# Kernel optimization log

Measured on AMD Instinct MI355X. Metric: run time of the kernel, lower is better.

The kernel has to match this reference:

```python
import jax, jax.numpy as jnp
import numpy as np

B, S, HID = 1, 2048, 2048
NH, NKV, HD = 16, 4, 128
ROPE_BASE = 10000.0


def _rope(q, k, positions):
    # q: [B,NH,S,HD], k: [B,NKV,S,HD]; rotate-half RoPE
    half = HD // 2
    inv_freq = 1.0 / (ROPE_BASE ** (jnp.arange(half, dtype=jnp.float32) / half))
    ang = positions.astype(jnp.float32)[:, None] * inv_freq  # [S, half]
    cos, sin = jnp.cos(ang), jnp.sin(ang)

    def apply(x):
        x1, x2 = x[..., :half], x[..., half:]
        return jnp.concatenate([x1 * cos - x2 * sin, x1 * sin + x2 * cos], axis=-1)

    return apply(q), apply(k)


def setup_inputs() -> dict:
    key = jax.random.key(0)
    ks = jax.random.split(key, 5)
    hidden_states = jax.random.normal(ks[0], (B, S, HID), dtype=jnp.float32)
    positions = jnp.arange(S, dtype=jnp.int32)
    # additive causal mask (finite large negative instead of -inf)
    mask = jnp.triu(jnp.full((S, S), -1e9, dtype=jnp.float32), k=1)[None, None]
    scale = 0.02
    Wq = jax.random.normal(ks[1], (HID, NH * HD), dtype=jnp.float32) * scale
    Wk = jax.random.normal(ks[2], (HID, NKV * HD), dtype=jnp.float32) * scale
    Wv = jax.random.normal(ks[3], (HID, NKV * HD), dtype=jnp.float32) * scale
    Wo = jax.random.normal(ks[4], (NH * HD, HID), dtype=jnp.float32) * scale
    return {"hidden_states": hidden_states, "positions": positions, "mask": mask,
            "Wq": Wq, "Wk": Wk, "Wv": Wv, "Wo": Wo}


def reference(hidden_states, positions, mask, Wq, Wk, Wv, Wo):
    groups = NH // NKV
    q = (hidden_states @ Wq).reshape(B, S, NH, HD).transpose(0, 2, 1, 3)
    k = (hidden_states @ Wk).reshape(B, S, NKV, HD).transpose(0, 2, 1, 3)
    v = (hidden_states @ Wv).reshape(B, S, NKV, HD).transpose(0, 2, 1, 3)
    q, k = _rope(q, k, positions)
    # GQA: duplicate kv heads (repeat_interleave along head dim)
    k = jnp.repeat(k, groups, axis=1)
    v = jnp.repeat(v, groups, axis=1)
    scale = 1.0 / jnp.sqrt(jnp.float32(HD))
    scores = jnp.einsum('bhqd,bhkd->bhqk', q, k) * scale + mask
    attn = jax.nn.softmax(scores.astype(jnp.float32), axis=-1).astype(q.dtype)
    out = jnp.einsum('bhqk,bhkd->bhqd', attn, v)
    out = out.transpose(0, 2, 1, 3).reshape(B, S, NH * HD)
    output = out @ Wo
    return (output, k, v)
```

## Files before the change

kernel.cpp:

```cpp
#include <hip/hip_runtime.h>
#include <hip/hip_bf16.h>
#include <math.h>

#define S_LEN 2048
#define HID_DIM 2048
#define NH 16
#define NKV 4
#define HD 128

typedef __attribute__((ext_vector_type(8))) short bf16x8;
typedef __attribute__((ext_vector_type(4))) float f32x4;

#define AS1 __attribute__((address_space(1)))
#define AS3 __attribute__((address_space(3)))

__device__ inline unsigned short f2bf(float f) {
  unsigned int u = __float_as_uint(f);
  unsigned int r = u + 0x7FFFu + ((u >> 16) & 1u);
  return (unsigned short)(r >> 16);
}
__device__ inline float bf2f(unsigned short u) {
  return __uint_as_float(((unsigned int)u) << 16);
}

__global__ __launch_bounds__(256) void transpose_all(
    const float* __restrict__ Wq, const float* __restrict__ Wk,
    const float* __restrict__ Wv, const float* __restrict__ Wo,
    unsigned short* __restrict__ WT, unsigned short* __restrict__ WoT,
    const float* __restrict__ hidden, unsigned short* __restrict__ h_bf)
{
  const int z = blockIdx.z;
  if (z == 4) {
    int bb = blockIdx.y * 64 + blockIdx.x;
    int t = threadIdx.y * 32 + threadIdx.x;
    int i = (bb * 256 + t) * 4;
    float4 v = *(const float4*)&hidden[i];
    ushort4 o;
    o.x = f2bf(v.x); o.y = f2bf(v.y); o.z = f2bf(v.z); o.w = f2bf(v.w);
    *(ushort4*)&h_bf[i] = o;
    return;
  }
  __shared__ float t[32][33];
  const float* W; unsigned short* D; int N;
  if (z == 0)      { W = Wq; D = WT;                          N = 2048; }
  else if (z == 1) { W = Wk; D = WT + (size_t)2048 * 2048;    N = 512;  }
  else if (z == 2) { W = Wv; D = WT + (size_t)2560 * 2048;    N = 512;  }
  else             { W = Wo; D = WoT;                         N = 2048; }
  int bx = blockIdx.x * 32;
  if (bx >= N) return;
  int by = blockIdx.y * 32;
  int tx = threadIdx.x, ty = threadIdx.y;
  #pragma unroll
  for (int i = 0; i < 32; i += 8)
    t[ty + i][tx] = W[(size_t)(by + ty + i) * N + bx + tx];
  __syncthreads();
  #pragma unroll
  for (int i = 0; i < 32; i += 8)
    D[(size_t)(bx + ty + i) * 2048 + by + tx] = f2bf(t[tx][ty + i]);
}

__global__ __launch_bounds__(512) void gemm_bt_8phase(
    const unsigned short* __restrict__ A,
    const unsigned short* __restrict__ Bt,
    unsigned short* __restrict__ P,
    int M, int N, int KF, int ksplit)
{
  extern __shared__ unsigned short smem[];
  unsigned short* Ab = smem;
  unsigned short* Bb = smem + 32768;
  const int bm = blockIdx.y * 256, bn = blockIdx.x * 256, z = blockIdx.z;
  const int Kh = KF / ksplit, k0z = z * Kh;
  const int NT = Kh >> 6;
  const int tid = threadIdx.x, lane = tid & 63, wave = tid >> 6;
  const int wm = wave >> 2, wn = wave & 3;
  const int quad = lane >> 4, lcol = lane & 15;

  auto stageA = [&](int t, int kh) {
    const unsigned short* src = A + (size_t)bm * KF + k0z + t * 64 + kh * 32;
    unsigned short* dst = Ab + (((t & 1) * 2 + kh) << 13);
    #pragma unroll
    for (int i = 0; i < 2; i++) {
      int s = i * 512 + tid;
      int row = s >> 2, dc = s & 3, g = dc ^ ((row >> 1) & 3);
      __builtin_amdgcn_global_load_lds(
          (const AS1 void*)(src + (size_t)row * KF + g * 8),
          (AS3 void*)(dst + s * 8), 16, 0, 0);
    }
  };
  auto stageB = [&](int t, int kh) {
    const unsigned short* src = Bt + (size_t)bn * KF + k0z + t * 64 + kh * 32;
    unsigned short* dst = Bb + (((t & 1) * 2 + kh) << 13);
    #pragma unroll
    for (int i = 0; i < 2; i++) {
      int s = i * 512 + tid;
      int row = s >> 2, dc = s & 3, g = dc ^ ((row >> 1) & 3);
      __builtin_amdgcn_global_load_lds(
          (const AS1 void*)(src + (size_t)row * KF + g * 8),
          (AS3 void*)(dst + s * 8), 16, 0, 0);
    }
  };
  auto ldA = [&](int cur, int kh, int mh, bf16x8* af) {
    const unsigned short* base = Ab + ((cur * 2 + kh) << 13);
    #pragma unroll
    for (int m = 0; m < 4; m++) {
      int row = wm * 128 + (mh * 4 + m) * 16 + lcol;
      int ch = quad ^ ((row >> 1) & 3);
      af[m] = *(const bf16x8*)&base[row * 32 + ch * 8];
    }
  };
  auto ldB = [&](int cur, int kh, bf16x8* bfr) {
    const unsigned short* base = Bb + ((cur * 2 + kh) << 13);
    #pragma unroll
    for (int n = 0; n < 4; n++) {
      int row = wn * 64 + n * 16 + lcol;
      int ch = quad ^ ((row >> 1) & 3);
      bfr[n] = *(const bf16x8*)&base[row * 32 + ch * 8];
    }
  };

  f32x4 zero = {0.f, 0.f, 0.f, 0.f};
  f32x4 acc[8][4];
  #pragma unroll
  for (int i = 0; i < 8; i++)
    #pragma unroll
    for (int j = 0; j < 4; j++) acc[i][j] = zero;

  stageA(0, 0); stageB(0, 0); stageA(0, 1); stageB(0, 1);
  if (NT > 1) { stageA(1, 0); stageB(1, 0); }
  asm volatile("s_waitcnt vmcnt(8)" ::: "memory");
  __builtin_amdgcn_s_barrier();

  for (int t = 0; t < NT; t++) {
    const int cur = t & 1;
    bf16x8 af[4], bfr[4];
    ldB(cur, 0, bfr);
    ldA(cur, 0, 0, af);
    __builtin_amdgcn_s_barrier();
    if (t + 1 < NT) stageA(t + 1, 1);
    __builtin_amdgcn_s_setprio(1);
    #pragma unroll
    for (int m = 0; m < 4; m++)
      #pragma unroll
      for (int n = 0; n < 4; n++)
        acc[m][n] = __builtin_amdgcn_mfma_f32_16x16x32_bf16(af[m], bfr[n], acc[m][n], 0, 0, 0);
    __builtin_amdgcn_s_setprio(0);
    ldA(cur, 0, 1, af);
    asm volatile("s_waitcnt vmcnt(6)" ::: "memory");
    __builtin_amdgcn_s_barrier();
    if (t + 1 < NT) stageB(t + 1, 1);
    __builtin_amdgcn_s_setprio(1);
    #pragma unroll
    for (int m = 0; m < 4; m++)
      #pragma unroll
      for (int n = 0; n < 4; n++)
        acc[4 + m][n] = __builtin_amdgcn_mfma_f32_16x16x32_bf16(af[m], bfr[n], acc[4 + m][n], 0, 0, 0);
    __builtin_amdgcn_s_setprio(0);
    ldB(cur, 1, bfr);
    ldA(cur, 1, 0, af);
    __builtin_amdgcn_s_barrier();
    if (t + 2 < NT) stageA(t + 2, 0);
    __builtin_amdgcn_s_setprio(1);
    #pragma unroll
    for (int m = 0; m < 4; m++)
      #pragma unroll
      for (int n = 0; n < 4; n++)
        acc[m][n] = __builtin_amdgcn_mfma_f32_16x16x32_bf16(af[m], bfr[n], acc[m][n], 0, 0, 0);
    __builtin_amdgcn_s_setprio(0);
    ldA(cur, 1, 1, af);
    asm volatile("s_waitcnt vmcnt(6)" ::: "memory");
    __builtin_amdgcn_s_barrier();
    if (t + 2 < NT) stageB(t + 2, 0);
    __builtin_amdgcn_s_setprio(1);
    #pragma unroll
    for (int m = 0; m < 4; m++)
      #pragma unroll
      for (int n = 0; n < 4; n++)
        acc[4 + m][n] = __builtin_amdgcn_mfma_f32_16x16x32_bf16(af[m], bfr[n], acc[4 + m][n], 0, 0, 0);
    __builtin_amdgcn_s_setprio(0);
  }

  unsigned short* Pz = P + (size_t)z * M * N;
  #pragma unroll
  for (int mr = 0; mr < 8; mr++)
    #pragma unroll
    for (int nr = 0; nr < 4; nr++)
      #pragma unroll
      for (int r = 0; r < 4; r++) {
        int mm = bm + wm * 128 + mr * 16 + quad * 4 + r;
        int nn = bn + wn * 64 + nr * 16 + lcol;
        Pz[(size_t)mm * N + nn] = f2bf(acc[mr][nr][r]);
      }
}

__global__ __launch_bounds__(256) void add_out_kernel(
    const unsigned short* __restrict__ P0, const unsigned short* __restrict__ P1,
    float* __restrict__ out, int n)
{
  int i = (blockIdx.x * 256 + threadIdx.x) * 8;
  if (i < n) {
    uint4 a = *(const uint4*)&P0[i];
    uint4 b = *(const uint4*)&P1[i];
    float4 o0, o1;
    o0.x = __uint_as_float(a.x << 16) + __uint_as_float(b.x << 16);
    o0.y = __uint_as_float(a.x & 0xFFFF0000u) + __uint_as_float(b.x & 0xFFFF0000u);
    o0.z = __uint_as_float(a.y << 16) + __uint_as_float(b.y << 16);
    o0.w = __uint_as_float(a.y & 0xFFFF0000u) + __uint_as_float(b.y & 0xFFFF0000u);
    o1.x = __uint_as_float(a.z << 16) + __uint_as_float(b.z << 16);
    o1.y = __uint_as_float(a.z & 0xFFFF0000u) + __uint_as_float(b.z & 0xFFFF0000u);
    o1.z = __uint_as_float(a.w << 16) + __uint_as_float(b.w << 16);
    o1.w = __uint_as_float(a.w & 0xFFFF0000u) + __uint_as_float(b.w & 0xFFFF0000u);
    *(float4*)&out[i] = o0;
    *(float4*)&out[i + 4] = o1;
  }
}

__global__ __launch_bounds__(256) void add_out4_kernel(
    const unsigned short* __restrict__ P0, const unsigned short* __restrict__ P1,
    const unsigned short* __restrict__ P2, const unsigned short* __restrict__ P3,
    float* __restrict__ out, int n)
{
  int i = (blockIdx.x * 256 + threadIdx.x) * 8;
  if (i < n) {
    uint4 a = *(const uint4*)&P0[i];
    uint4 b = *(const uint4*)&P1[i];
    uint4 c = *(const uint4*)&P2[i];
    uint4 d = *(const uint4*)&P3[i];
    float o[8];
    o[0] = __uint_as_float(a.x << 16) + __uint_as_float(b.x << 16)
         + __uint_as_float(c.x << 16) + __uint_as_float(d.x << 16);
    o[1] = __uint_as_float(a.x & 0xFFFF0000u) + __uint_as_float(b.x & 0xFFFF0000u)
         + __uint_as_float(c.x & 0xFFFF0000u) + __uint_as_float(d.x & 0xFFFF0000u);
    o[2] = __uint_as_float(a.y << 16) + __uint_as_float(b.y << 16)
         + __uint_as_float(c.y << 16) + __uint_as_float(d.y << 16);
    o[3] = __uint_as_float(a.y & 0xFFFF0000u) + __uint_as_float(b.y & 0xFFFF0000u)
         + __uint_as_float(c.y & 0xFFFF0000u) + __uint_as_float(d.y & 0xFFFF0000u);
    o[4] = __uint_as_float(a.z << 16) + __uint_as_float(b.z << 16)
         + __uint_as_float(c.z << 16) + __uint_as_float(d.z << 16);
    o[5] = __uint_as_float(a.z & 0xFFFF0000u) + __uint_as_float(b.z & 0xFFFF0000u)
         + __uint_as_float(c.z & 0xFFFF0000u) + __uint_as_float(d.z & 0xFFFF0000u);
    o[6] = __uint_as_float(a.w << 16) + __uint_as_float(b.w << 16)
         + __uint_as_float(c.w << 16) + __uint_as_float(d.w << 16);
    o[7] = __uint_as_float(a.w & 0xFFFF0000u) + __uint_as_float(b.w & 0xFFFF0000u)
         + __uint_as_float(c.w & 0xFFFF0000u) + __uint_as_float(d.w & 0xFFFF0000u);
    *(float4*)&out[i] = *(float4*)&o[0];
    *(float4*)&out[i + 4] = *(float4*)&o[4];
  }
}

__global__ __launch_bounds__(256) void rope_prepv_kernel(
    const unsigned short* __restrict__ P0,
    const unsigned short* __restrict__ P1,
    const int* __restrict__ positions,
    unsigned short* __restrict__ q_ws,
    unsigned short* __restrict__ k_ws,
    float* __restrict__ outk,
    float* __restrict__ outv,
    unsigned short* __restrict__ vT)
{
  __shared__ float t[32][33];
  if (blockIdx.x < 2048) {
    const float QSCALE = 0.08838834764831845f * 1.4426950408889634f;
    int s = blockIdx.x;
    float pos = (float)positions[s];
    const unsigned short* r0 = &P0[(size_t)s * 3072];
    const unsigned short* r1 = &P1[(size_t)s * 3072];
    int tt = threadIdx.y * 32 + threadIdx.x;
    int j = tt & 63, grp = tt >> 6;
    float freq = expf(-(float)j * 0.14391156831212787f);
    float ang = pos * freq;
    float sn, c;
    sincosf(ang, &sn, &c);
    #pragma unroll
    for (int ci = 0; ci < 5; ci++) {
      int ch = grp * 5 + ci;
      if (ch < NH) {
        int i1 = ch * HD + j, i2 = i1 + 64;
        float x1 = bf2f(r0[i1]) + bf2f(r1[i1]);
        float x2 = bf2f(r0[i2]) + bf2f(r1[i2]);
        float o1 = x1 * c - x2 * sn;
        float o2 = x1 * sn + x2 * c;
        size_t base = ((size_t)ch * S_LEN + s) * HD;
        q_ws[base + j] = f2bf(o1 * QSCALE);
        q_ws[base + j + 64] = f2bf(o2 * QSCALE);
      } else {
        int kv = ch - NH;
        int i1 = 2048 + kv * HD + j, i2 = i1 + 64;
        float x1 = bf2f(r0[i1]) + bf2f(r1[i1]);
        float x2 = bf2f(r0[i2]) + bf2f(r1[i2]);
        float o1 = x1 * c - x2 * sn;
        float o2 = x1 * sn + x2 * c;
        size_t kbase = ((size_t)kv * S_LEN + s) * HD;
        k_ws[kbase + j] = f2bf(o1);
        k_ws[kbase + j + 64] = f2bf(o2);
        #pragma unroll
        for (int g = 0; g < 4; g++) {
          size_t ob = ((size_t)(kv * 4 + g) * S_LEN + s) * HD;
          outk[ob + j] = o1;
          outk[ob + j + 64] = o2;
        }
      }
    }
  } else {
    int b = blockIdx.x - 2048;
    int s0 = (b & 63) * 32, d0 = ((b >> 6) & 3) * 32, kv = b >> 8;
    int tx = threadIdx.x & 31, ty = (threadIdx.y * 32 + threadIdx.x) >> 5;
    #pragma unroll
    for (int i = 0; i < 32; i += 8) {
      size_t idx = (size_t)(s0 + ty + i) * 3072 + 2560 + kv * HD + d0 + tx;
      t[ty + i][tx] = bf2f(P0[idx]) + bf2f(P1[idx]);
    }
    __syncthreads();
    #pragma unroll
    for (int i = 0; i < 32; i += 8) {
      float val = t[ty + i][tx];
      #pragma unroll
      for (int g = 0; g < 4; g++)
        outv[((size_t)(kv * 4 + g) * S_LEN + s0 + ty + i) * HD + d0 + tx] = val;
    }
    #pragma unroll
    for (int i = 0; i < 32; i += 8)
      vT[((size_t)kv * HD + d0 + ty + i) * S_LEN + s0 + tx] = f2bf(t[tx][ty + i]);
  }
}

__device__ inline void stage_k_tile(const unsigned short* kbase, unsigned short* dst,
                                    int wave, int lane) {
  #pragma unroll
  for (int i = 0; i < 4; i++) {
    int row = wave * 16 + i * 4 + (lane >> 4);
    int c = (lane & 15) ^ (row & 7);
    __builtin_amdgcn_global_load_lds(
        (const AS1 void*)(kbase + (size_t)row * HD + c * 8),
        (AS3 void*)(dst + (wave * 16 + i * 4) * 128),
        16, 0, 0);
  }
}

__device__ inline void stage_v_tile(const unsigned short* vbase, unsigned short* dst,
                                    int wave, int lane) {
  #pragma unroll
  for (int i = 0; i < 4; i++) {
    int row = wave * 32 + i * 8 + (lane >> 3);
    int c = (lane & 7) ^ (row & 7);
    __builtin_amdgcn_global_load_lds(
        (const AS1 void*)(vbase + (size_t)row * S_LEN + c * 8),
        (AS3 void*)(dst + (wave * 32 + i * 8) * 64),
        16, 0, 0);
  }
}

#define PLD 72
#define C2F 23.082320654223414f

__global__ __launch_bounds__(256) void flash_attn3(
    const unsigned short* __restrict__ q_ws,
    const unsigned short* __restrict__ k_ws,
    const unsigned short* __restrict__ vT_ws,
    unsigned short* __restrict__ attn_ws)
{
  __shared__ __align__(16) unsigned short Ks[2][64 * 128];
  __shared__ __align__(16) unsigned short Vs[128 * 64];
  __shared__ __align__(16) unsigned short Ps[4][16 * PLD];
  const int b = blockIdx.x;
  const int u = b >> 4, h = b & 15, kvh = h >> 2;
  const int qt = (u < 16) ? (31 - u) : (u - 16);
  const int tid = threadIdx.x, lane = tid & 63, wave = tid >> 6;
  const int quad = lane >> 4, lcol = lane & 15;
  const int qrow = qt * 64 + wave * 16 + lcol;

  const unsigned short* kh = k_ws + (size_t)kvh * S_LEN * HD;
  const unsigned short* vh = vT_ws + (size_t)kvh * HD * S_LEN;

  bf16x8 qf[4];
  {
    const unsigned short* qp = &q_ws[((size_t)h * S_LEN + qrow) * HD + quad * 8];
    #pragma unroll
    for (int st = 0; st < 4; st++) qf[st] = *(const bf16x8*)&qp[st * 32];
  }
  f32x4 zero = {0.f, 0.f, 0.f, 0.f};
  f32x4 o_acc[8];
  #pragma unroll
  for (int i = 0; i < 8; i++) o_acc[i] = zero;
  float l_acc = 0.f;

  stage_k_tile(kh, &Ks[0][0], wave, lane);

  for (int kt = 0; kt <= qt; kt++) {
    int cur = kt & 1;
    __syncthreads();
    stage_v_tile(vh + kt * 64, &Vs[0], wave, lane);
    if (kt < qt) stage_k_tile(kh + (size_t)(kt + 1) * 64 * HD, &Ks[cur ^ 1][0], wave, lane);

    f32x4 sc[4];
    #pragma unroll
    for (int kb = 0; kb < 4; kb++) {
      sc[kb] = zero;
      #pragma unroll
      for (int st = 0; st < 4; st++) {
        int krow = kb * 16 + lcol;
        bf16x8 kf = *(const bf16x8*)&Ks[cur][krow * 128 + (((st * 4 + quad) ^ (lcol & 7)) * 8)];
        sc[kb] = __builtin_amdgcn_mfma_f32_16x16x32_bf16(kf, qf[st], sc[kb], 0, 0, 0);
      }
    }

    float pv[4][4];
    if (kt < qt) {
      #pragma unroll
      for (int kb = 0; kb < 4; kb++)
        #pragma unroll
        for (int r = 0; r < 4; r++) {
          float p = exp2f(sc[kb][r] - C2F);
          pv[kb][r] = p;
          l_acc += p;
        }
    } else {
      #pragma unroll
      for (int kb = 0; kb < 4; kb++)
        #pragma unroll
        for (int r = 0; r < 4; r++) {
          int key = kt * 64 + kb * 16 + quad * 4 + r;
          float p = (key <= qrow) ? exp2f(sc[kb][r] - C2F) : 0.f;
          pv[kb][r] = p;
          l_acc += p;
        }
    }

    unsigned short* myPs = &Ps[wave][0];
    #pragma unroll
    for (int kb = 0; kb < 4; kb++) {
      unsigned int u0 = (__float_as_uint(pv[kb][0]) + 0x8000u) >> 16;
      unsigned int u1 = (__float_as_uint(pv[kb][1]) + 0x8000u) & 0xFFFF0000u;
      unsigned int u2 = (__float_as_uint(pv[kb][2]) + 0x8000u) >> 16;
      unsigned int u3 = (__float_as_uint(pv[kb][3]) + 0x8000u) & 0xFFFF0000u;
      uint2 w2; w2.x = u0 | u1; w2.y = u2 | u3;
      *(uint2*)&myPs[lcol * PLD + kb * 16 + quad * 4] = w2;
    }
    __syncthreads();

    bf16x8 pa0 = *(const bf16x8*)&myPs[lcol * PLD + quad * 8];
    bf16x8 pa1 = *(const bf16x8*)&myPs[lcol * PLD + 32 + quad * 8];
    #pragma unroll
    for (int ob = 0; ob < 8; ob++) {
      int vrow = ob * 16 + lcol, sw = lcol & 7;
      bf16x8 v0 = *(const bf16x8*)&Vs[vrow * 64 + ((quad ^ sw) * 8)];
      bf16x8 v1 = *(const bf16x8*)&Vs[vrow * 64 + (((quad + 4) ^ sw) * 8)];
      o_acc[ob] = __builtin_amdgcn_mfma_f32_16x16x32_bf16(pa0, v0, o_acc[ob], 0, 0, 0);
      o_acc[ob] = __builtin_amdgcn_mfma_f32_16x16x32_bf16(pa1, v1, o_acc[ob], 0, 0, 0);
    }
  }

  float l = l_acc;
  l += __shfl_xor(l, 16);
  l += __shfl_xor(l, 32);
  float l_t[4];
  #pragma unroll
  for (int r = 0; r < 4; r++)
    l_t[r] = __shfl(l, (lane & 48) + quad * 4 + r);
  #pragma unroll
  for (int r = 0; r < 4; r++) {
    float inv = 1.f / l_t[r];
    int row = qt * 64 + wave * 16 + quad * 4 + r;
    #pragma unroll
    for (int ob = 0; ob < 8; ob++)
      attn_ws[(size_t)row * (NH * HD) + h * HD + ob * 16 + lcol] = f2bf(o_acc[ob][r] * inv);
  }
}

extern "C" void kernel_launch(void* const* d_in, const int* in_sizes, int n_in,
                              void* d_out, int out_size, void* d_ws, size_t ws_size,
                              hipStream_t stream)
{
  const float* hidden    = (const float*)d_in[0];
  const int*   positions = (const int*)d_in[1];
  const float* Wq = (const float*)d_in[3];
  const float* Wk = (const float*)d_in[4];
  const float* Wv = (const float*)d_in[5];
  const float* Wo = (const float*)d_in[6];

  float* out  = (float*)d_out;
  float* outk = out + (size_t)S_LEN * HID_DIM;
  float* outv = outk + (size_t)NH * S_LEN * HD;

  char* ws = (char*)d_ws;
  unsigned short* h_bf   = (unsigned short*)(ws);
  unsigned short* WT     = (unsigned short*)(ws + ((size_t)8  << 20));
  unsigned short* WoT    = (unsigned short*)(ws + ((size_t)20 << 20));
  unsigned short* qkvP   = (unsigned short*)(ws + ((size_t)28 << 20));
  unsigned short* q_ws   = (unsigned short*)(ws + ((size_t)52 << 20));
  unsigned short* k_ws   = (unsigned short*)(ws + ((size_t)60 << 20));
  unsigned short* vT_ws  = (unsigned short*)(ws + ((size_t)62 << 20));
  unsigned short* attn   = (unsigned short*)(ws + ((size_t)64 << 20));
  unsigned short* qkvP1  = qkvP + (size_t)S_LEN * 3072;
  unsigned short* outP   = qkvP;
  const size_t OPE = (size_t)2048 * 2048;

  transpose_all<<<dim3(64, 64, 5), dim3(32, 8), 0, stream>>>(
      Wq, Wk, Wv, Wo, WT, WoT, hidden, h_bf);

  gemm_bt_8phase<<<dim3(12, 8, 2), 512, 131072, stream>>>(h_bf, WT, qkvP, 2048, 3072, 2048, 2);

  rope_prepv_kernel<<<3072, 256, 0, stream>>>(qkvP, qkvP1, positions,
                                              q_ws, k_ws, outk, outv, vT_ws);

  flash_attn3<<<dim3(512), 256, 0, stream>>>(q_ws, k_ws, vT_ws, attn);

  gemm_bt_8phase<<<dim3(8, 8, 4), 512, 131072, stream>>>(attn, WoT, outP, 2048, 2048, 2048, 4);
  add_out4_kernel<<<2048, 256, 0, stream>>>(outP, outP + OPE, outP + 2 * OPE, outP + 3 * OPE,
                                            out, S_LEN * HID_DIM);
}
```

Measured before the change: 237.3 us.

## Process two 16-row query slabs per wave in flash attention with 128-thread blocks

The flash attention kernel now runs 2 waves per block instead of 4, and each wave handles 32 query rows as two 16-row slabs. Each K fragment read from LDS feeds two MFMAs, and each V fragment feeds four, which halves LDS reads per MFMA. The trade-off is more accumulator registers and fewer waves per block to hide load and barrier latency. Staging loops double their trip count to keep the same tile sizes, and the unused add_out_kernel is removed.

```diff
diff --git a/kernel.cpp b/kernel.cpp
--- a/kernel.cpp
+++ b/kernel.cpp
@@ -190,28 +190,6 @@
         int nn = bn + wn * 64 + nr * 16 + lcol;
         Pz[(size_t)mm * N + nn] = f2bf(acc[mr][nr][r]);
       }
-}
-
-__global__ __launch_bounds__(256) void add_out_kernel(
-    const unsigned short* __restrict__ P0, const unsigned short* __restrict__ P1,
-    float* __restrict__ out, int n)
-{
-  int i = (blockIdx.x * 256 + threadIdx.x) * 8;
-  if (i < n) {
-    uint4 a = *(const uint4*)&P0[i];
-    uint4 b = *(const uint4*)&P1[i];
-    float4 o0, o1;
-    o0.x = __uint_as_float(a.x << 16) + __uint_as_float(b.x << 16);
-    o0.y = __uint_as_float(a.x & 0xFFFF0000u) + __uint_as_float(b.x & 0xFFFF0000u);
-    o0.z = __uint_as_float(a.y << 16) + __uint_as_float(b.y << 16);
-    o0.w = __uint_as_float(a.y & 0xFFFF0000u) + __uint_as_float(b.y & 0xFFFF0000u);
-    o1.x = __uint_as_float(a.z << 16) + __uint_as_float(b.z << 16);
-    o1.y = __uint_as_float(a.z & 0xFFFF0000u) + __uint_as_float(b.z & 0xFFFF0000u);
-    o1.z = __uint_as_float(a.w << 16) + __uint_as_float(b.w << 16);
-    o1.w = __uint_as_float(a.w & 0xFFFF0000u) + __uint_as_float(b.w & 0xFFFF0000u);
-    *(float4*)&out[i] = o0;
-    *(float4*)&out[i + 4] = o1;
-  }
 }
 
 __global__ __launch_bounds__(256) void add_out4_kernel(
@@ -323,28 +301,28 @@
   }
 }
 
-__device__ inline void stage_k_tile(const unsigned short* kbase, unsigned short* dst,
-                                    int wave, int lane) {
-  #pragma unroll
-  for (int i = 0; i < 4; i++) {
-    int row = wave * 16 + i * 4 + (lane >> 4);
+__device__ inline void stage_k_tile2(const unsigned short* kbase, unsigned short* dst,
+                                     int wave, int lane) {
+  #pragma unroll
+  for (int i = 0; i < 8; i++) {
+    int row = wave * 32 + i * 4 + (lane >> 4);
     int c = (lane & 15) ^ (row & 7);
     __builtin_amdgcn_global_load_lds(
         (const AS1 void*)(kbase + (size_t)row * HD + c * 8),
-        (AS3 void*)(dst + (wave * 16 + i * 4) * 128),
+        (AS3 void*)(dst + (wave * 32 + i * 4) * 128),
         16, 0, 0);
   }
 }
 
-__device__ inline void stage_v_tile(const unsigned short* vbase, unsigned short* dst,
-                                    int wave, int lane) {
-  #pragma unroll
-  for (int i = 0; i < 4; i++) {
-    int row = wave * 32 + i * 8 + (lane >> 3);
+__device__ inline void stage_v_tile2(const unsigned short* vbase, unsigned short* dst,
+                                     int wave, int lane) {
+  #pragma unroll
+  for (int i = 0; i < 8; i++) {
+    int row = wave * 64 + i * 8 + (lane >> 3);
     int c = (lane & 7) ^ (row & 7);
     __builtin_amdgcn_global_load_lds(
         (const AS1 void*)(vbase + (size_t)row * S_LEN + c * 8),
-        (AS3 void*)(dst + (wave * 32 + i * 8) * 64),
+        (AS3 void*)(dst + (wave * 64 + i * 8) * 64),
         16, 0, 0);
   }
 }
@@ -352,7 +330,7 @@
 #define PLD 72
 #define C2F 23.082320654223414f
 
-__global__ __launch_bounds__(256) void flash_attn3(
+__global__ __launch_bounds__(128) void flash_attn7(
     const unsigned short* __restrict__ q_ws,
     const unsigned short* __restrict__ k_ws,
     const unsigned short* __restrict__ vT_ws,
@@ -366,103 +344,129 @@
   const int qt = (u < 16) ? (31 - u) : (u - 16);
   const int tid = threadIdx.x, lane = tid & 63, wave = tid >> 6;
   const int quad = lane >> 4, lcol = lane & 15;
-  const int qrow = qt * 64 + wave * 16 + lcol;
+  const int qrow0 = qt * 64 + wave * 32 + lcol;
+  const int qrow1 = qrow0 + 16;
 
   const unsigned short* kh = k_ws + (size_t)kvh * S_LEN * HD;
   const unsigned short* vh = vT_ws + (size_t)kvh * HD * S_LEN;
 
-  bf16x8 qf[4];
-  {
-    const unsigned short* qp = &q_ws[((size_t)h * S_LEN + qrow) * HD + quad * 8];
-    #pragma unroll
-    for (int st = 0; st < 4; st++) qf[st] = *(const bf16x8*)&qp[st * 32];
+  bf16x8 qf[2][4];
+  #pragma unroll
+  for (int r = 0; r < 2; r++) {
+    const unsigned short* qp =
+        &q_ws[((size_t)h * S_LEN + qt * 64 + wave * 32 + r * 16 + lcol) * HD + quad * 8];
+    #pragma unroll
+    for (int st = 0; st < 4; st++) qf[r][st] = *(const bf16x8*)&qp[st * 32];
   }
   f32x4 zero = {0.f, 0.f, 0.f, 0.f};
-  f32x4 o_acc[8];
-  #pragma unroll
-  for (int i = 0; i < 8; i++) o_acc[i] = zero;
-  float l_acc = 0.f;
-
-  stage_k_tile(kh, &Ks[0][0], wave, lane);
+  f32x4 o_acc[2][8];
+  #pragma unroll
+  for (int r = 0; r < 2; r++)
+    #pragma unroll
+    for (int i = 0; i < 8; i++) o_acc[r][i] = zero;
+  float l_acc[2] = {0.f, 0.f};
+
+  stage_k_tile2(kh, &Ks[0][0], wave, lane);
 
   for (int kt = 0; kt <= qt; kt++) {
     int cur = kt & 1;
     __syncthreads();
-    stage_v_tile(vh + kt * 64, &Vs[0], wave, lane);
-    if (kt < qt) stage_k_tile(kh + (size_t)(kt + 1) * 64 * HD, &Ks[cur ^ 1][0], wave, lane);
-
-    f32x4 sc[4];
+    stage_v_tile2(vh + kt * 64, &Vs[0], wave, lane);
+    if (kt < qt) stage_k_tile2(kh + (size_t)(kt + 1) * 64 * HD, &Ks[cur ^ 1][0], wave, lane);
+
+    f32x4 sc[2][4];
     #pragma unroll
     for (int kb = 0; kb < 4; kb++) {
-      sc[kb] = zero;
+      sc[0][kb] = zero;
+      sc[1][kb] = zero;
       #pragma unroll
       for (int st = 0; st < 4; st++) {
         int krow = kb * 16 + lcol;
         bf16x8 kf = *(const bf16x8*)&Ks[cur][krow * 128 + (((st * 4 + quad) ^ (lcol & 7)) * 8)];
-        sc[kb] = __builtin_amdgcn_mfma_f32_16x16x32_bf16(kf, qf[st], sc[kb], 0, 0, 0);
+        sc[0][kb] = __builtin_amdgcn_mfma_f32_16x16x32_bf16(kf, qf[0][st], sc[0][kb], 0, 0, 0);
+        sc[1][kb] = __builtin_amdgcn_mfma_f32_16x16x32_bf16(kf, qf[1][st], sc[1][kb], 0, 0, 0);
       }
     }
 
-    float pv[4][4];
+    float pv[2][4][4];
     if (kt < qt) {
       #pragma unroll
-      for (int kb = 0; kb < 4; kb++)
+      for (int r = 0; r < 2; r++)
         #pragma unroll
-        for (int r = 0; r < 4; r++) {
-          float p = exp2f(sc[kb][r] - C2F);
-          pv[kb][r] = p;
-          l_acc += p;
-        }
+        for (int kb = 0; kb < 4; kb++)
+          #pragma unroll
+          for (int rr = 0; rr < 4; rr++) {
+            float p = exp2f(sc[r][kb][rr] - C2F);
+            pv[r][kb][rr] = p;
+            l_acc[r] += p;
+          }
     } else {
       #pragma unroll
-      for (int kb = 0; kb < 4; kb++)
+      for (int r = 0; r < 2; r++) {
+        int qr = (r == 0) ? qrow0 : qrow1;
         #pragma unroll
-        for (int r = 0; r < 4; r++) {
-          int key = kt * 64 + kb * 16 + quad * 4 + r;
-          float p = (key <= qrow) ? exp2f(sc[kb][r] - C2F) : 0.f;
-          pv[kb][r] = p;
-          l_acc += p;
-        }
-    }
-
-    unsigned short* myPs = &Ps[wave][0];
-    #pragma unroll
-    for (int kb = 0; kb < 4; kb++) {
-      unsigned int u0 = (__float_as_uint(pv[kb][0]) + 0x8000u) >> 16;
-      unsigned int u1 = (__float_as_uint(pv[kb][1]) + 0x8000u) & 0xFFFF0000u;
-      unsigned int u2 = (__float_as_uint(pv[kb][2]) + 0x8000u) >> 16;
-      unsigned int u3 = (__float_as_uint(pv[kb][3]) + 0x8000u) & 0xFFFF0000u;
-      uint2 w2; w2.x = u0 | u1; w2.y = u2 | u3;
-      *(uint2*)&myPs[lcol * PLD + kb * 16 + quad * 4] = w2;
+        for (int kb = 0; kb < 4; kb++)
+          #pragma unroll
+          for (int rr = 0; rr < 4; rr++) {
+            int key = kt * 64 + kb * 16 + quad * 4 + rr;
+            float p = (key <= qr) ? exp2f(sc[r][kb][rr] - C2F) : 0.f;
+            pv[r][kb][rr] = p;
+            l_acc[r] += p;
+          }
+      }
+    }
+
+    #pragma unroll
+    for (int r = 0; r < 2; r++) {
+      unsigned short* myPs = &Ps[wave * 2 + r][0];
+      #pragma unroll
+      for (int kb = 0; kb < 4; kb++) {
+        unsigned int u0 = (__float_as_uint(pv[r][kb][0]) + 0x8000u) >> 16;
+        unsigned int u1 = (__float_as_uint(pv[r][kb][1]) + 0x8000u) & 0xFFFF0000u;
+        unsigned int u2 = (__float_as_uint(pv[r][kb][2]) + 0x8000u) >> 16;
+        unsigned int u3 = (__float_as_uint(pv[r][kb][3]) + 0x8000u) & 0xFFFF0000u;
+        uint2 w2; w2.x = u0 | u1; w2.y = u2 | u3;
+        *(uint2*)&myPs[lcol * PLD + kb * 16 + quad * 4] = w2;
+      }
     }
     __syncthreads();
 
-    bf16x8 pa0 = *(const bf16x8*)&myPs[lcol * PLD + quad * 8];
-    bf16x8 pa1 = *(const bf16x8*)&myPs[lcol * PLD + 32 + quad * 8];
+    bf16x8 pa0[2], pa1[2];
+    #pragma unroll
+    for (int r = 0; r < 2; r++) {
+      const unsigned short* myPs = &Ps[wave * 2 + r][0];
+      pa0[r] = *(const bf16x8*)&myPs[lcol * PLD + quad * 8];
+      pa1[r] = *(const bf16x8*)&myPs[lcol * PLD + 32 + quad * 8];
+    }
     #pragma unroll
     for (int ob = 0; ob < 8; ob++) {
       int vrow = ob * 16 + lcol, sw = lcol & 7;
       bf16x8 v0 = *(const bf16x8*)&Vs[vrow * 64 + ((quad ^ sw) * 8)];
       bf16x8 v1 = *(const bf16x8*)&Vs[vrow * 64 + (((quad + 4) ^ sw) * 8)];
-      o_acc[ob] = __builtin_amdgcn_mfma_f32_16x16x32_bf16(pa0, v0, o_acc[ob], 0, 0, 0);
-      o_acc[ob] = __builtin_amdgcn_mfma_f32_16x16x32_bf16(pa1, v1, o_acc[ob], 0, 0, 0);
-    }
-  }
-
-  float l = l_acc;
-  l += __shfl_xor(l, 16);
-  l += __shfl_xor(l, 32);
-  float l_t[4];
-  #pragma unroll
-  for (int r = 0; r < 4; r++)
-    l_t[r] = __shfl(l, (lane & 48) + quad * 4 + r);
-  #pragma unroll
-  for (int r = 0; r < 4; r++) {
-    float inv = 1.f / l_t[r];
-    int row = qt * 64 + wave * 16 + quad * 4 + r;
-    #pragma unroll
-    for (int ob = 0; ob < 8; ob++)
-      attn_ws[(size_t)row * (NH * HD) + h * HD + ob * 16 + lcol] = f2bf(o_acc[ob][r] * inv);
+      o_acc[0][ob] = __builtin_amdgcn_mfma_f32_16x16x32_bf16(pa0[0], v0, o_acc[0][ob], 0, 0, 0);
+      o_acc[0][ob] = __builtin_amdgcn_mfma_f32_16x16x32_bf16(pa1[0], v1, o_acc[0][ob], 0, 0, 0);
+      o_acc[1][ob] = __builtin_amdgcn_mfma_f32_16x16x32_bf16(pa0[1], v0, o_acc[1][ob], 0, 0, 0);
+      o_acc[1][ob] = __builtin_amdgcn_mfma_f32_16x16x32_bf16(pa1[1], v1, o_acc[1][ob], 0, 0, 0);
+    }
+  }
+
+  #pragma unroll
+  for (int r = 0; r < 2; r++) {
+    float l = l_acc[r];
+    l += __shfl_xor(l, 16);
+    l += __shfl_xor(l, 32);
+    float l_t[4];
+    #pragma unroll
+    for (int rr = 0; rr < 4; rr++)
+      l_t[rr] = __shfl(l, (lane & 48) + quad * 4 + rr);
+    #pragma unroll
+    for (int rr = 0; rr < 4; rr++) {
+      float inv = 1.f / l_t[rr];
+      int row = qt * 64 + wave * 32 + r * 16 + quad * 4 + rr;
+      #pragma unroll
+      for (int ob = 0; ob < 8; ob++)
+        attn_ws[(size_t)row * (NH * HD) + h * HD + ob * 16 + lcol] = f2bf(o_acc[r][ob][rr] * inv);
+    }
   }
 }
 
@@ -502,7 +506,7 @@
   rope_prepv_kernel<<<3072, 256, 0, stream>>>(qkvP, qkvP1, positions,
                                               q_ws, k_ws, outk, outv, vT_ws);
 
-  flash_attn3<<<dim3(512), 256, 0, stream>>>(q_ws, k_ws, vT_ws, attn);
+  flash_attn7<<<dim3(512), 128, 0, stream>>>(q_ws, k_ws, vT_ws, attn);
 
   gemm_bt_8phase<<<dim3(8, 8, 4), 512, 131072, stream>>>(attn, WoT, outP, 2048, 2048, 2048, 4);
   add_out4_kernel<<<2048, 256, 0, stream>>>(outP, outP + OPE, outP + 2 * OPE, outP + 3 * OPE,
```

Result: slower. 255.0 us (+7.4%).
